# Kernel optimization log

Measured on AMD Instinct MI355X. Metric: run time of the kernel, lower is better.

Reference implementation:

```python
import jax, jax.numpy as jnp
import numpy as np

B, S, HID, H = 1, 1024, 4096, 32
DH = HID // H          # 128 head dim
DL = 2048 // H         # 64 low-rank dim per head
K = 63                 # causal conv kernel along query axis
NLAYERS = 3            # num_deep_cnn_layers
EPS = 1e-5
ROPE_BASE = 10000.0


def _layernorm(x, w, b):
    m = x.mean(-1, keepdims=True)
    v = x.var(-1, keepdims=True)
    return (x - m) * jax.lax.rsqrt(v + EPS) * w + b


def setup_inputs() -> dict:
    key = jax.random.key(0)
    ks = jax.random.split(key, 12)
    s = 0.02
    causal = jnp.tril(jnp.ones((S, S), dtype=bool))
    neg = jnp.finfo(jnp.float32).min
    return {
        "hidden_states": jax.random.normal(ks[0], (B, S, HID), jnp.float32),
        "attention_mask": jnp.broadcast_to(jnp.where(causal, 0.0, neg)[None, None], (B, 1, S, S)),
        "position_ids": jnp.broadcast_to(jnp.arange(S, dtype=jnp.int32)[None, :], (B, S)),
        "Wq": jax.random.normal(ks[1], (HID, HID), jnp.float32) * s,
        "Wk": jax.random.normal(ks[2], (HID, HID), jnp.float32) * s,
        "Wv": jax.random.normal(ks[3], (HID, HID), jnp.float32) * s,
        "Wo": jax.random.normal(ks[4], (HID, HID), jnp.float32) * s,
        "Wdq": jax.random.normal(ks[5], (DL, DH), jnp.float32) * s,  # attn_down_proj_q weight
        "Wdk": jax.random.normal(ks[6], (DL, DH), jnp.float32) * s,  # attn_down_proj_k weight
        "ln1_w": jnp.ones((S,), jnp.float32), "ln1_b": jnp.zeros((S,), jnp.float32),
        "ln2_w": jnp.ones((S,), jnp.float32), "ln2_b": jnp.zeros((S,), jnp.float32),
        "conv_w": jax.random.normal(ks[7], (NLAYERS, H, 1, K, 1), jnp.float32) / np.sqrt(K),
        "conv_b": jnp.zeros((NLAYERS, H), jnp.float32),
        "scaler_w": jax.random.normal(ks[8], (1, S), jnp.float32) * s,
        "scaler_b": jnp.zeros((1,), jnp.float32),
    }


def reference(hidden_states, attention_mask, position_ids, Wq, Wk, Wv, Wo, Wdq, Wdk,
              ln1_w, ln1_b, ln2_w, ln2_b, conv_w, conv_b, scaler_w, scaler_b):
    bsz, q_len, _ = hidden_states.shape

    def heads(x):
        return x.reshape(bsz, q_len, H, DH).transpose(0, 2, 1, 3)  # [B,H,S,DH]

    q = heads(hidden_states @ Wq.T)
    k = heads(hidden_states @ Wk.T)
    v = heads(hidden_states @ Wv.T)

    # rotary embeddings (LLaMA-style rotate_half)
    inv_freq = 1.0 / (ROPE_BASE ** (jnp.arange(0, DH, 2, dtype=jnp.float32) / DH))
    freqs = jnp.outer(jnp.arange(q_len, dtype=jnp.float32), inv_freq)
    emb = jnp.concatenate([freqs, freqs], axis=-1)             # [S,DH]
    cos = jnp.cos(emb)[position_ids][:, None]                  # [B,1,S,DH]
    sin = jnp.sin(emb)[position_ids][:, None]

    def rope(x):
        x1, x2 = jnp.split(x, 2, axis=-1)
        return x * cos + jnp.concatenate([-x2, x1], axis=-1) * sin

    q, k = rope(q), rope(k)

    # low-rank down-projection of q/k
    ql = jnp.einsum('bhsd,ed->bhse', q, Wdq)
    kl = jnp.einsum('bhsd,ed->bhse', k, Wdk)

    attn = jnp.einsum('bhqe,bhke->bhqk', ql, kl) / jnp.sqrt(jnp.float32(DL))  # [B,H,S,S]
    est_scale = jnp.einsum('bhqk,ok->bhqo', attn, scaler_w) + scaler_b       # [B,H,S,1]

    # CNN score predictor: LN -> (causal depthwise conv + ReLU) x NLAYERS -> LN
    x = _layernorm(attn, ln1_w, ln1_b)
    for i in range(NLAYERS):
        x = jax.lax.conv_general_dilated(
            x, conv_w[i], window_strides=(1, 1),
            padding=[(K - 1, 0), (0, 0)],  # causal along query axis
            dimension_numbers=('NCHW', 'OIHW', 'NCHW'),
            feature_group_count=H)
        x = jax.nn.relu(x + conv_b[i][None, :, None, None])
    x = _layernorm(x, ln2_w, ln2_b)

    x = x + attention_mask
    x = jnp.maximum(x, jnp.finfo(x.dtype).min)
    p = jax.nn.softmax(x.astype(jnp.float32), axis=-1).astype(hidden_states.dtype)
    p = p * jax.nn.sigmoid(est_scale)

    out = jnp.einsum('bhqk,bhkd->bhqd', p, v)
    out = out.transpose(0, 2, 1, 3).reshape(bsz, q_len, HID)
    return out @ Wo.T
```

## Files before the change

### kernel.cpp

```cpp
#include <hip/hip_runtime.h>
#include <hip/hip_bf16.h>

typedef __attribute__((ext_vector_type(8))) short bf16x8;
typedef __attribute__((ext_vector_type(4))) float f32x4;

#define TILE 64
#define TK 16

__device__ inline short f2bf(float x) {
    unsigned u = __float_as_uint(x);
    unsigned r = (u + 0x7fffu + ((u >> 16) & 1u)) >> 16;
    return (short)r;
}
__device__ inline float bf2f(short h) {
    return __uint_as_float(((unsigned)(unsigned short)h) << 16);
}

template<bool BT>
__global__ __launch_bounds__(256)
void gemm_f32(const float* __restrict__ A, int lda, long sA,
              const float* __restrict__ B, int ldb, long sB,
              float* __restrict__ C, int ldc, long sC,
              int M, int N, int Kd, float alpha)
{
    long bz = blockIdx.z;
    A += bz * sA; B += bz * sB; C += bz * sC;
    int m0 = blockIdx.y * TILE, n0 = blockIdx.x * TILE;
    __shared__ float As[TK][TILE + 4];
    __shared__ float Bs[TK][TILE + 4];
    int tid = threadIdx.x;
    int tm = (tid >> 4) * 4;
    int tn = (tid & 15) * 4;
    float acc[4][4] = {};
    for (int k0 = 0; k0 < Kd; k0 += TK) {
        {
            int kk = tid & 15;
            int m  = tid >> 4;
            #pragma unroll
            for (int mm = 0; mm < 4; ++mm)
                As[kk][m + mm * 16] = A[(long)(m0 + m + mm * 16) * lda + k0 + kk];
        }
        {
            int kk = tid & 15;
            int n  = tid >> 4;
            #pragma unroll
            for (int nn = 0; nn < 4; ++nn)
                Bs[kk][n + nn * 16] = B[(long)(n0 + n + nn * 16) * ldb + k0 + kk];
        }
        __syncthreads();
        #pragma unroll
        for (int kk = 0; kk < TK; ++kk) {
            float4 a4 = *reinterpret_cast<const float4*>(&As[kk][tm]);
            float4 b4 = *reinterpret_cast<const float4*>(&Bs[kk][tn]);
            float a[4] = {a4.x, a4.y, a4.z, a4.w};
            float b[4] = {b4.x, b4.y, b4.z, b4.w};
            #pragma unroll
            for (int i = 0; i < 4; ++i)
                #pragma unroll
                for (int j = 0; j < 4; ++j)
                    acc[i][j] += a[i] * b[j];
        }
        __syncthreads();
    }
    #pragma unroll
    for (int i = 0; i < 4; ++i)
        #pragma unroll
        for (int j = 0; j < 4; ++j)
            C[(long)(m0 + tm + i) * ldc + n0 + tn + j] = alpha * acc[i][j];
}

__device__ inline void gld_lds16(const __hip_bfloat16* g, __hip_bfloat16* l)
{
    __builtin_amdgcn_global_load_lds(
        (const __attribute__((address_space(1))) unsigned int*)g,
        (__attribute__((address_space(3))) unsigned int*)l,
        16, 0, 0);
}

template<int CMODE>
__global__ __launch_bounds__(256)
void gemm16(const __hip_bfloat16* __restrict__ A, int lda, long sA,
            const __hip_bfloat16* __restrict__ B, int ldb, long sB,
            void* __restrict__ Cv, int ldc, long sC,
            int Kd, float alpha)
{
    __shared__ __hip_bfloat16 As[128][32];
    __shared__ __hip_bfloat16 Bs[128][32];
    long bz = blockIdx.z;
    A += bz * sA; B += bz * sB;
    int m0 = blockIdx.y * 128, n0 = blockIdx.x * 128;
    int tid  = threadIdx.x;
    int w    = tid >> 6, lane = tid & 63;
    int wm   = w >> 1,  wn   = w & 1;
    int lrow = lane >> 2;
    int lseg = (lane & 3) * 8;
    int fr   = lane & 15;
    int kg   = (lane >> 4) * 8;
    f32x4 acc[4][4] = {};
    for (int k0 = 0; k0 < Kd; k0 += 32) {
        #pragma unroll
        for (int i = 0; i < 2; ++i) {
            int r = w * 32 + i * 16;
            gld_lds16(&A[(long)(m0 + r + lrow) * lda + k0 + lseg], &As[r][0]);
            gld_lds16(&B[(long)(n0 + r + lrow) * ldb + k0 + lseg], &Bs[r][0]);
        }
        __syncthreads();
        bf16x8 af[4], bfr[4];
        #pragma unroll
        for (int m = 0; m < 4; ++m)
            af[m] = *(const bf16x8*)&As[wm * 64 + m * 16 + fr][kg];
        #pragma unroll
        for (int n = 0; n < 4; ++n)
            bfr[n] = *(const bf16x8*)&Bs[wn * 64 + n * 16 + fr][kg];
        #pragma unroll
        for (int m = 0; m < 4; ++m)
            #pragma unroll
            for (int n = 0; n < 4; ++n)
                acc[m][n] = __builtin_amdgcn_mfma_f32_16x16x32_bf16(af[m], bfr[n], acc[m][n], 0, 0, 0);
        __syncthreads();
    }
    int crow0 = (lane >> 4) * 4;
    if constexpr (CMODE == 2) {
        __hip_bfloat16* CT = (__hip_bfloat16*)Cv + bz * sC;
        #pragma unroll
        for (int m = 0; m < 4; ++m)
            #pragma unroll
            for (int n = 0; n < 4; ++n)
                #pragma unroll
                for (int r = 0; r < 4; ++r) {
                    int row = m0 + wm * 64 + m * 16 + crow0 + r;
                    int col = n0 + wn * 64 + n * 16 + fr;
                    CT[(long)col * ldc + row] = __float2bfloat16(alpha * acc[m][n][r]);
                }
    } else {
        float* C = (float*)Cv + bz * sC;
        #pragma unroll
        for (int m = 0; m < 4; ++m)
            #pragma unroll
            for (int n = 0; n < 4; ++n)
                #pragma unroll
                for (int r = 0; r < 4; ++r) {
                    long idx = (long)(m0 + wm * 64 + m * 16 + crow0 + r) * ldc
                             + n0 + wn * 64 + n * 16 + fr;
                    float v = alpha * acc[m][n][r];
                    if constexpr (CMODE == 1) v += C[idx];
                    C[idx] = v;
                }
    }
}

__global__ __launch_bounds__(256)
void gemm16_sk(const __hip_bfloat16* __restrict__ A0, const __hip_bfloat16* __restrict__ A1,
               const __hip_bfloat16* __restrict__ A2, int lda,
               const __hip_bfloat16* __restrict__ B0, const __hip_bfloat16* __restrict__ B1,
               const __hip_bfloat16* __restrict__ B2, int ldb,
               float* __restrict__ C, int ldc,
               int kSteps, int chunksPerTerm, float alpha)
{
    __shared__ __hip_bfloat16 As[128][32];
    __shared__ __hip_bfloat16 Bs[128][32];
    int z    = blockIdx.z;
    int term = z / chunksPerTerm;
    int sub  = z - term * chunksPerTerm;
    const __hip_bfloat16* A = (term == 0) ? A0 : (term == 1) ? A1 : A2;
    const __hip_bfloat16* B = (term == 0) ? B0 : (term == 1) ? B1 : B2;
    int kbase = sub * kSteps * 32;
    int m0 = blockIdx.y * 128, n0 = blockIdx.x * 128;
    int tid  = threadIdx.x;
    int w    = tid >> 6, lane = tid & 63;
    int wm   = w >> 1,  wn   = w & 1;
    int lrow = lane >> 2;
    int lseg = (lane & 3) * 8;
    int fr   = lane & 15;
    int kg   = (lane >> 4) * 8;
    f32x4 acc[4][4] = {};
    for (int it = 0; it < kSteps; ++it) {
        int k0 = kbase + it * 32;
        #pragma unroll
        for (int i = 0; i < 2; ++i) {
            int r = w * 32 + i * 16;
            gld_lds16(&A[(long)(m0 + r + lrow) * lda + k0 + lseg], &As[r][0]);
            gld_lds16(&B[(long)(n0 + r + lrow) * ldb + k0 + lseg], &Bs[r][0]);
        }
        __syncthreads();
        bf16x8 af[4], bfr[4];
        #pragma unroll
        for (int m = 0; m < 4; ++m)
            af[m] = *(const bf16x8*)&As[wm * 64 + m * 16 + fr][kg];
        #pragma unroll
        for (int n = 0; n < 4; ++n)
            bfr[n] = *(const bf16x8*)&Bs[wn * 64 + n * 16 + fr][kg];
        #pragma unroll
        for (int m = 0; m < 4; ++m)
            #pragma unroll
            for (int n = 0; n < 4; ++n)
                acc[m][n] = __builtin_amdgcn_mfma_f32_16x16x32_bf16(af[m], bfr[n], acc[m][n], 0, 0, 0);
        __syncthreads();
    }
    int crow0 = (lane >> 4) * 4;
    #pragma unroll
    for (int m = 0; m < 4; ++m)
        #pragma unroll
        for (int n = 0; n < 4; ++n)
            #pragma unroll
            for (int r = 0; r < 4; ++r) {
                long idx = (long)(m0 + wm * 64 + m * 16 + crow0 + r) * ldc
                         + n0 + wn * 64 + n * 16 + fr;
                atomicAdd(&C[idx], alpha * acc[m][n][r]);
            }
}

#define LP 40
__global__ __launch_bounds__(256)
void gemm_s(const float* __restrict__ A, int lda, long sA,
            const float* __restrict__ B, int ldb, long sB,
            float* __restrict__ C, int ldc, long sC,
            int Kd, float alpha)
{
    __shared__ short Ah[128][LP];
    __shared__ short Bh[128][LP];
    __shared__ short Al[128][LP];
    __shared__ short Bl[128][LP];
    long bz = blockIdx.z;
    A += bz * sA; B += bz * sB; C += bz * sC;
    int m0 = blockIdx.y * 128, n0 = blockIdx.x * 128;
    int tid  = threadIdx.x;
    int lane = tid & 63;
    int w    = tid >> 6;
    int wm   = w >> 1, wn = w & 1;
    int srow = tid >> 1;
    int scol = (tid & 1) * 16;
    int fr   = lane & 15;
    int kg   = (lane >> 4) * 8;
    f32x4 acc[4][4] = {};
    for (int k0 = 0; k0 < Kd; k0 += 32) {
        #pragma unroll
        for (int ab = 0; ab < 2; ++ab) {
            const float* src = ab ? (B + (long)(n0 + srow) * ldb + k0 + scol)
                                  : (A + (long)(m0 + srow) * lda + k0 + scol);
            short* dh = ab ? &Bh[srow][scol] : &Ah[srow][scol];
            short* dl = ab ? &Bl[srow][scol] : &Al[srow][scol];
            #pragma unroll
            for (int half = 0; half < 2; ++half) {
                float4 x0 = *reinterpret_cast<const float4*>(src + half * 8);
                float4 x1 = *reinterpret_cast<const float4*>(src + half * 8 + 4);
                float xs[8] = {x0.x, x0.y, x0.z, x0.w, x1.x, x1.y, x1.z, x1.w};
                bf16x8 hv, lv;
                #pragma unroll
                for (int j = 0; j < 8; ++j) {
                    short hb = f2bf(xs[j]);
                    hv[j] = hb;
                    lv[j] = f2bf(xs[j] - bf2f(hb));
                }
                *reinterpret_cast<bf16x8*>(dh + half * 8) = hv;
                *reinterpret_cast<bf16x8*>(dl + half * 8) = lv;
            }
        }
        __syncthreads();
        bf16x8 afh[4], bfh[4], afl[4], bfl[4];
        #pragma unroll
        for (int m = 0; m < 4; ++m) {
            afh[m] = *(const bf16x8*)&Ah[wm * 64 + m * 16 + fr][kg];
            afl[m] = *(const bf16x8*)&Al[wm * 64 + m * 16 + fr][kg];
        }
        #pragma unroll
        for (int n = 0; n < 4; ++n) {
            bfh[n] = *(const bf16x8*)&Bh[wn * 64 + n * 16 + fr][kg];
            bfl[n] = *(const bf16x8*)&Bl[wn * 64 + n * 16 + fr][kg];
        }
        #pragma unroll
        for (int m = 0; m < 4; ++m)
            #pragma unroll
            for (int n = 0; n < 4; ++n) {
                acc[m][n] = __builtin_amdgcn_mfma_f32_16x16x32_bf16(afh[m], bfh[n], acc[m][n], 0, 0, 0);
                acc[m][n] = __builtin_amdgcn_mfma_f32_16x16x32_bf16(afh[m], bfl[n], acc[m][n], 0, 0, 0);
                acc[m][n] = __builtin_amdgcn_mfma_f32_16x16x32_bf16(afl[m], bfh[n], acc[m][n], 0, 0, 0);
            }
        __syncthreads();
    }
    int crow0 = (lane >> 4) * 4;
    #pragma unroll
    for (int m = 0; m < 4; ++m)
        #pragma unroll
        for (int n = 0; n < 4; ++n)
            #pragma unroll
            for (int r = 0; r < 4; ++r)
                C[(long)(m0 + wm * 64 + m * 16 + crow0 + r) * ldc
                  + n0 + wn * 64 + n * 16 + fr] = alpha * acc[m][n][r];
}

struct alignas(8) s4 { short a, b, c, d; };
template<bool LO>
__global__ __launch_bounds__(256)
void cvt_part(const float* __restrict__ x, short* __restrict__ y, long n4)
{
    long i = (long)blockIdx.x * 256 + threadIdx.x;
    long stride = (long)gridDim.x * 256;
    for (; i < n4; i += stride) {
        float4 v = reinterpret_cast<const float4*>(x)[i];
        float xs[4] = {v.x, v.y, v.z, v.w};
        s4 o;
        short* op = &o.a;
        #pragma unroll
        for (int j = 0; j < 4; ++j) {
            short hb = f2bf(xs[j]);
            op[j] = LO ? f2bf(xs[j] - bf2f(hb)) : hb;
        }
        reinterpret_cast<s4*>(y)[i] = o;
    }
}

__global__ __launch_bounds__(256)
void cvt_both(const float* __restrict__ x, short* __restrict__ yh,
              short* __restrict__ yl, long n4)
{
    long i = (long)blockIdx.x * 256 + threadIdx.x;
    long stride = (long)gridDim.x * 256;
    for (; i < n4; i += stride) {
        float4 v = reinterpret_cast<const float4*>(x)[i];
        float xs[4] = {v.x, v.y, v.z, v.w};
        s4 oh, ol;
        short* hp = &oh.a; short* lp = &ol.a;
        #pragma unroll
        for (int j = 0; j < 4; ++j) {
            short hb = f2bf(xs[j]);
            hp[j] = hb;
            lp[j] = f2bf(xs[j] - bf2f(hb));
        }
        reinterpret_cast<s4*>(yh)[i] = oh;
        reinterpret_cast<s4*>(yl)[i] = ol;
    }
}

__global__ __launch_bounds__(256)
void rope_kernel(float* __restrict__ q, float* __restrict__ k, const int* __restrict__ pos)
{
    int i = blockIdx.x * 256 + threadIdx.x;
    if (i >= 1024 * 32 * 64) return;
    int d   = i & 63;
    int rem = i >> 6;
    int h   = rem & 31;
    int s   = rem >> 5;
    float p = (float)pos[s];
    float inv = exp2f(-(float)d * (13.287712379549449f / 64.0f));
    float ang = p * inv;
    float c = cosf(ang), sn = sinf(ang);
    long base = ((long)s * 4096) + h * 128 + d;
    float x1 = q[base], x2 = q[base + 64];
    q[base]      = x1 * c - x2 * sn;
    q[base + 64] = x2 * c + x1 * sn;
    x1 = k[base]; x2 = k[base + 64];
    k[base]      = x1 * c - x2 * sn;
    k[base + 64] = x2 * c + x1 * sn;
}

__global__ __launch_bounds__(256)
void est_ln1(const float* __restrict__ x, float* __restrict__ y,
             const float* __restrict__ sw, const float* __restrict__ sbias,
             float* __restrict__ est,
             const float* __restrict__ w, const float* __restrict__ b)
{
    long row = blockIdx.x;
    const float* xr = x + row * 1024;
    float* yr = y + row * 1024;
    __shared__ float sb[12];
    float v[4];
    float s = 0.f, ss = 0.f, dt = 0.f;
    #pragma unroll
    for (int i = 0; i < 4; ++i) {
        int c = threadIdx.x + i * 256;
        v[i] = xr[c];
        s += v[i]; ss += v[i] * v[i]; dt += v[i] * sw[c];
    }
    #pragma unroll
    for (int off = 32; off; off >>= 1) {
        s  += __shfl_down(s, off, 64);
        ss += __shfl_down(ss, off, 64);
        dt += __shfl_down(dt, off, 64);
    }
    int wid = threadIdx.x >> 6, lane = threadIdx.x & 63;
    if (!lane) { sb[wid] = s; sb[4 + wid] = ss; sb[8 + wid] = dt; }
    __syncthreads();
    s  = sb[0] + sb[1] + sb[2] + sb[3];
    ss = sb[4] + sb[5] + sb[6] + sb[7];
    if (threadIdx.x == 0) est[row] = sb[8] + sb[9] + sb[10] + sb[11] + sbias[0];
    float mean = s * (1.f / 1024.f);
    float var  = ss * (1.f / 1024.f) - mean * mean;
    float inv  = rsqrtf(var + 1e-5f);
    #pragma unroll
    for (int i = 0; i < 4; ++i) {
        int c = threadIdx.x + i * 256;
        yr[c] = (v[i] - mean) * inv * w[c] + b[c];
    }
}

__global__ __launch_bounds__(256)
void conv_fast(const float* __restrict__ x, float* __restrict__ y,
               const float* __restrict__ cw, const float* __restrict__ cb,
               int layer, int h0)
{
    const int S = 1024;
    int h  = blockIdx.z;
    int hg = h0 + h;
    int q0 = blockIdx.y * 64;
    int k0 = blockIdx.x * 64;
    __shared__ float ws[63];
    if (threadIdx.x < 63) ws[threadIdx.x] = cw[(layer * 32 + hg) * 63 + threadIdx.x];
    __syncthreads();
    int c   = threadIdx.x & 63;
    int grp = threadIdx.x >> 6;
    int qb  = q0 + grp * 16;
    const float* xh = x + (long)h * S * S + k0 + c;
    float X[78];
    #pragma unroll
    for (int j = 0; j < 78; ++j) {
        int g = qb - 62 + j;
        X[j] = (g >= 0) ? xh[(long)g * S] : 0.f;
    }
    float wr[63];
    #pragma unroll
    for (int t = 0; t < 63; ++t) wr[t] = ws[t];
    float bias = cb[layer * 32 + hg];
    float* yh = y + (long)h * S * S + k0 + c;
    #pragma unroll
    for (int i = 0; i < 16; ++i) {
        float a0 = 0.f, a1 = 0.f, a2 = 0.f, a3 = 0.f;
        #pragma unroll
        for (int t = 0; t < 60; t += 4) {
            a0 += wr[t]     * X[i + t];
            a1 += wr[t + 1] * X[i + t + 1];
            a2 += wr[t + 2] * X[i + t + 2];
            a3 += wr[t + 3] * X[i + t + 3];
        }
        a0 += wr[60] * X[i + 60];
        a1 += wr[61] * X[i + 61];
        a2 += wr[62] * X[i + 62];
        float acc = bias + ((a0 + a1) + (a2 + a3));
        yh[(long)(qb + i) * S] = fmaxf(acc, 0.f);
    }
}

__global__ __launch_bounds__(256)
void ln2_softmax(const float* __restrict__ x, __hip_bfloat16* __restrict__ pb,
                 const float* __restrict__ w, const float* __restrict__ b,
                 const float* __restrict__ mask, const float* __restrict__ est)
{
    const int S = 1024;
    long row = blockIdx.x;
    int q = (int)(row & (S - 1));
    const float* xr = x + row * 1024;
    const float* mrow = mask + (long)q * S;
    __shared__ float sb[8];
    float v[4];
    float s = 0.f, ss = 0.f;
    #pragma unroll
    for (int i = 0; i < 4; ++i) {
        int c = threadIdx.x + i * 256;
        v[i] = xr[c];
        s += v[i]; ss += v[i] * v[i];
    }
    #pragma unroll
    for (int off = 32; off; off >>= 1) {
        s  += __shfl_down(s, off, 64);
        ss += __shfl_down(ss, off, 64);
    }
    int wid = threadIdx.x >> 6, lane = threadIdx.x & 63;
    if (!lane) { sb[wid] = s; sb[4 + wid] = ss; }
    __syncthreads();
    s  = sb[0] + sb[1] + sb[2] + sb[3];
    ss = sb[4] + sb[5] + sb[6] + sb[7];
    float mean = s * (1.f / 1024.f);
    float var  = ss * (1.f / 1024.f) - mean * mean;
    float inv  = rsqrtf(var + 1e-5f);
    const float FMIN = -3.4028235e38f;
    float mx = FMIN;
    #pragma unroll
    for (int i = 0; i < 4; ++i) {
        int c = threadIdx.x + i * 256;
        float t = (v[i] - mean) * inv * w[c] + b[c] + mrow[c];
        t = fmaxf(t, FMIN);
        v[i] = t;
        mx = fmaxf(mx, t);
    }
    #pragma unroll
    for (int off = 32; off; off >>= 1) mx = fmaxf(mx, __shfl_down(mx, off, 64));
    __syncthreads();
    if (!lane) sb[wid] = mx;
    __syncthreads();
    mx = fmaxf(fmaxf(sb[0], sb[1]), fmaxf(sb[2], sb[3]));
    float s2 = 0.f;
    #pragma unroll
    for (int i = 0; i < 4; ++i) { v[i] = expf(v[i] - mx); s2 += v[i]; }
    #pragma unroll
    for (int off = 32; off; off >>= 1) s2 += __shfl_down(s2, off, 64);
    __syncthreads();
    if (!lane) sb[4 + wid] = s2;
    __syncthreads();
    s2 = sb[4] + sb[5] + sb[6] + sb[7];
    float e = est[row];
    float sc = (1.f / (1.f + expf(-e))) / s2;
    __hip_bfloat16* pr = pb + row * S;
    #pragma unroll
    for (int i = 0; i < 4; ++i) {
        int c = threadIdx.x + i * 256;
        pr[c] = __float2bfloat16(v[i] * sc);
    }
}

extern "C" void kernel_launch(void* const* d_in, const int* in_sizes, int n_in,
                              void* d_out, int out_size, void* d_ws, size_t ws_size,
                              hipStream_t stream) {
    const int S = 1024, H = 32, HID = 4096, DH = 128, DL = 64;

    const float* hs   = (const float*)d_in[0];
    const float* mask = (const float*)d_in[1];
    const int*   pos  = (const int*)d_in[2];
    const float* Wq   = (const float*)d_in[3];
    const float* Wk   = (const float*)d_in[4];
    const float* Wv   = (const float*)d_in[5];
    const float* Wo   = (const float*)d_in[6];
    const float* Wdq  = (const float*)d_in[7];
    const float* Wdk  = (const float*)d_in[8];
    const float* ln1w = (const float*)d_in[9];
    const float* ln1b = (const float*)d_in[10];
    const float* ln2w = (const float*)d_in[11];
    const float* ln2b = (const float*)d_in[12];
    const float* cw   = (const float*)d_in[13];
    const float* cb   = (const float*)d_in[14];
    const float* sw   = (const float*)d_in[15];
    const float* sbia = (const float*)d_in[16];
    float* out = (float*)d_out;

    float* p   = (float*)d_ws;
    float* qb  = p; p += (long)S * HID;
    float* kb  = p; p += (long)S * HID;
    float* ql  = p; p += (long)H * S * DL;
    float* kl  = p; p += (long)H * S * DL;
    float* est = p; p += (long)H * S;
    short* hsH = (short*)p; p += (long)S * HID / 2;
    short* hsL = (short*)p; p += (long)S * HID / 2;
    short* Wb  = (short*)p; p += (long)HID * HID / 2;
    short* WbL = (short*)p; p += (long)HID * HID / 2;
    float* ao  = qb;
    short* aoH = hsH;
    short* vT  = hsL;

    long wsFloats  = (long)(ws_size / 4);
    long usedFixed = p - (float*)d_ws;
    long perHead   = 2L * S * S;
    int CH = (int)((wsFloats - usedFixed) / perHead);
    if (CH > H) CH = H;
    if (CH < 1) CH = 1;
    float* sc0 = p;
    float* sc1 = sc0 + (long)CH * S * S;
    __hip_bfloat16* pb = (__hip_bfloat16*)sc1;

    dim3 blk(256);
    long n4_hs = (long)S * HID / 4, n4_W = (long)HID * HID / 4;
    size_t projBytes = (size_t)S * HID * sizeof(float);

    cvt_both<<<2048, blk, 0, stream>>>(hs, hsH, hsL, n4_hs);

    hipMemsetAsync(qb, 0, projBytes, stream);
    cvt_both<<<2048, blk, 0, stream>>>(Wq, Wb, WbL, n4_W);
    gemm16_sk<<<dim3(HID / 128, S / 128, 6), blk, 0, stream>>>(
        (__hip_bfloat16*)hsH, (__hip_bfloat16*)hsL, (__hip_bfloat16*)hsH, HID,
        (__hip_bfloat16*)Wb,  (__hip_bfloat16*)Wb,  (__hip_bfloat16*)WbL, HID,
        qb, HID, 64, 2, 1.f);

    hipMemsetAsync(kb, 0, projBytes, stream);
    cvt_both<<<2048, blk, 0, stream>>>(Wk, Wb, WbL, n4_W);
    gemm16_sk<<<dim3(HID / 128, S / 128, 6), blk, 0, stream>>>(
        (__hip_bfloat16*)hsH, (__hip_bfloat16*)hsL, (__hip_bfloat16*)hsH, HID,
        (__hip_bfloat16*)Wb,  (__hip_bfloat16*)Wb,  (__hip_bfloat16*)WbL, HID,
        kb, HID, 64, 2, 1.f);

    cvt_part<false><<<2048, blk, 0, stream>>>(Wv, Wb, n4_W);
    gemm16<2><<<dim3(HID / 128, S / 128, 1), blk, 0, stream>>>(
        (__hip_bfloat16*)hsH, HID, 0, (__hip_bfloat16*)Wb, HID, 0, vT, S, 0, HID, 1.f);

    rope_kernel<<<(S * H * 64 + 255) / 256, blk, 0, stream>>>(qb, kb, pos);

    gemm_f32<true><<<dim3(1, S / 64, H), blk, 0, stream>>>(qb, HID, 128, Wdq, DH, 0, ql, DL, (long)S * DL, S, DL, DH, 1.f);
    gemm_f32<true><<<dim3(1, S / 64, H), blk, 0, stream>>>(kb, HID, 128, Wdk, DH, 0, kl, DL, (long)S * DL, S, DL, DH, 1.f);

    for (int c0 = 0; c0 < H; c0 += CH) {
        int ch = (c0 + CH <= H) ? CH : (H - c0);
        gemm_s<<<dim3(S / 128, S / 128, ch), blk, 0, stream>>>(
            ql + (long)c0 * S * DL, DL, (long)S * DL,
            kl + (long)c0 * S * DL, DL, (long)S * DL,
            sc0, S, (long)S * S, DL, 0.125f);
        est_ln1<<<ch * S, blk, 0, stream>>>(sc0, sc1, sw, sbia, est + (long)c0 * S, ln1w, ln1b);
        conv_fast<<<dim3(16, 16, ch), blk, 0, stream>>>(sc1, sc0, cw, cb, 0, c0);
        conv_fast<<<dim3(16, 16, ch), blk, 0, stream>>>(sc0, sc1, cw, cb, 1, c0);
        conv_fast<<<dim3(16, 16, ch), blk, 0, stream>>>(sc1, sc0, cw, cb, 2, c0);
        ln2_softmax<<<ch * S, blk, 0, stream>>>(sc0, pb, ln2w, ln2b, mask, est + (long)c0 * S);
        gemm16<0><<<dim3(1, S / 128, ch), blk, 0, stream>>>(
            (__hip_bfloat16*)pb, S, (long)S * S,
            (__hip_bfloat16*)(vT + (long)c0 * DH * S), S, (long)DH * S,
            ao + (long)c0 * 128, HID, 128,
            S, 1.f);
    }

    cvt_part<false><<<2048, blk, 0, stream>>>(ao, aoH, n4_hs);
    cvt_part<false><<<2048, blk, 0, stream>>>(Wo, Wb, n4_W);
    hipMemsetAsync(out, 0, projBytes, stream);
    gemm16_sk<<<dim3(HID / 128, S / 128, 2), blk, 0, stream>>>(
        (__hip_bfloat16*)aoH, (__hip_bfloat16*)aoH, (__hip_bfloat16*)aoH, HID,
        (__hip_bfloat16*)Wb,  (__hip_bfloat16*)Wb,  (__hip_bfloat16*)Wb,  HID,
        out, HID, 64, 2, 1.f);
}
```

Before: 1.147 ms.

## Split-K projections deeper, route V through split-K plus transpose, emit bf16 attention output

The Q/K projection split-K factor doubles, giving more K-chunks and more blocks. The V projection moves from a single-slice transposed-store GEMM to a split-K GEMM into fp32 followed by a new shared-memory transpose kernel. The P·V GEMM now writes bf16 directly through a new epilogue mode, which removes the separate fp32-to-bf16 conversion pass before the output projection. These changes aim to fill more CUs on the skinny GEMMs and cut a memory pass, in exchange for extra atomic accumulation traffic and one added transpose kernel.

```diff
diff --git a/kernel.cpp b/kernel.cpp
--- a/kernel.cpp
+++ b/kernel.cpp
@@ -132,6 +132,16 @@
                     int col = n0 + wn * 64 + n * 16 + fr;
                     CT[(long)col * ldc + row] = __float2bfloat16(alpha * acc[m][n][r]);
                 }
+    } else if constexpr (CMODE == 3) {
+        __hip_bfloat16* C = (__hip_bfloat16*)Cv + bz * sC;
+        #pragma unroll
+        for (int m = 0; m < 4; ++m)
+            #pragma unroll
+            for (int n = 0; n < 4; ++n)
+                #pragma unroll
+                for (int r = 0; r < 4; ++r)
+                    C[(long)(m0 + wm * 64 + m * 16 + crow0 + r) * ldc
+                      + n0 + wn * 64 + n * 16 + fr] = __float2bfloat16(alpha * acc[m][n][r]);
     } else {
         float* C = (float*)Cv + bz * sC;
         #pragma unroll
@@ -333,6 +343,20 @@
 }
 
 __global__ __launch_bounds__(256)
+void transpose_v(const float* __restrict__ v, __hip_bfloat16* __restrict__ vT)
+{
+    __shared__ __hip_bfloat16 t[64][65];
+    int h = blockIdx.z, s0 = blockIdx.x * 64, d0 = blockIdx.y * 64;
+    int c = threadIdx.x & 63, r = threadIdx.x >> 6;
+    for (int i = r; i < 64; i += 4)
+        t[i][c] = __float2bfloat16(v[(long)(s0 + i) * 4096 + h * 128 + d0 + c]);
+    __syncthreads();
+    __hip_bfloat16* o = vT + ((long)h * 128 + d0) * 1024 + s0;
+    for (int i = r; i < 64; i += 4)
+        o[(long)i * 1024 + c] = t[c][i];
+}
+
+__global__ __launch_bounds__(256)
 void rope_kernel(float* __restrict__ q, float* __restrict__ k, const int* __restrict__ pos)
 {
     int i = blockIdx.x * 256 + threadIdx.x;
@@ -541,7 +565,6 @@
     short* hsL = (short*)p; p += (long)S * HID / 2;
     short* Wb  = (short*)p; p += (long)HID * HID / 2;
     short* WbL = (short*)p; p += (long)HID * HID / 2;
-    float* ao  = qb;
     short* aoH = hsH;
     short* vT  = hsL;
 
@@ -563,26 +586,30 @@
 
     hipMemsetAsync(qb, 0, projBytes, stream);
     cvt_both<<<2048, blk, 0, stream>>>(Wq, Wb, WbL, n4_W);
-    gemm16_sk<<<dim3(HID / 128, S / 128, 6), blk, 0, stream>>>(
+    gemm16_sk<<<dim3(HID / 128, S / 128, 12), blk, 0, stream>>>(
         (__hip_bfloat16*)hsH, (__hip_bfloat16*)hsL, (__hip_bfloat16*)hsH, HID,
         (__hip_bfloat16*)Wb,  (__hip_bfloat16*)Wb,  (__hip_bfloat16*)WbL, HID,
-        qb, HID, 64, 2, 1.f);
+        qb, HID, 32, 4, 1.f);
 
     hipMemsetAsync(kb, 0, projBytes, stream);
     cvt_both<<<2048, blk, 0, stream>>>(Wk, Wb, WbL, n4_W);
-    gemm16_sk<<<dim3(HID / 128, S / 128, 6), blk, 0, stream>>>(
+    gemm16_sk<<<dim3(HID / 128, S / 128, 12), blk, 0, stream>>>(
         (__hip_bfloat16*)hsH, (__hip_bfloat16*)hsL, (__hip_bfloat16*)hsH, HID,
         (__hip_bfloat16*)Wb,  (__hip_bfloat16*)Wb,  (__hip_bfloat16*)WbL, HID,
-        kb, HID, 64, 2, 1.f);
-
-    cvt_part<false><<<2048, blk, 0, stream>>>(Wv, Wb, n4_W);
-    gemm16<2><<<dim3(HID / 128, S / 128, 1), blk, 0, stream>>>(
-        (__hip_bfloat16*)hsH, HID, 0, (__hip_bfloat16*)Wb, HID, 0, vT, S, 0, HID, 1.f);
+        kb, HID, 32, 4, 1.f);
 
     rope_kernel<<<(S * H * 64 + 255) / 256, blk, 0, stream>>>(qb, kb, pos);
 
     gemm_f32<true><<<dim3(1, S / 64, H), blk, 0, stream>>>(qb, HID, 128, Wdq, DH, 0, ql, DL, (long)S * DL, S, DL, DH, 1.f);
     gemm_f32<true><<<dim3(1, S / 64, H), blk, 0, stream>>>(kb, HID, 128, Wdk, DH, 0, kl, DL, (long)S * DL, S, DL, DH, 1.f);
+
+    hipMemsetAsync(qb, 0, projBytes, stream);
+    cvt_part<false><<<2048, blk, 0, stream>>>(Wv, Wb, n4_W);
+    gemm16_sk<<<dim3(HID / 128, S / 128, 4), blk, 0, stream>>>(
+        (__hip_bfloat16*)hsH, (__hip_bfloat16*)hsH, (__hip_bfloat16*)hsH, HID,
+        (__hip_bfloat16*)Wb,  (__hip_bfloat16*)Wb,  (__hip_bfloat16*)Wb,  HID,
+        qb, HID, 32, 4, 1.f);
+    transpose_v<<<dim3(S / 64, DH / 64, H), blk, 0, stream>>>(qb, (__hip_bfloat16*)vT);
 
     for (int c0 = 0; c0 < H; c0 += CH) {
         int ch = (c0 + CH <= H) ? CH : (H - c0);
@@ -595,18 +622,17 @@
         conv_fast<<<dim3(16, 16, ch), blk, 0, stream>>>(sc0, sc1, cw, cb, 1, c0);
         conv_fast<<<dim3(16, 16, ch), blk, 0, stream>>>(sc1, sc0, cw, cb, 2, c0);
         ln2_softmax<<<ch * S, blk, 0, stream>>>(sc0, pb, ln2w, ln2b, mask, est + (long)c0 * S);
-        gemm16<0><<<dim3(1, S / 128, ch), blk, 0, stream>>>(
+        gemm16<3><<<dim3(1, S / 128, ch), blk, 0, stream>>>(
             (__hip_bfloat16*)pb, S, (long)S * S,
             (__hip_bfloat16*)(vT + (long)c0 * DH * S), S, (long)DH * S,
-            ao + (long)c0 * 128, HID, 128,
+            aoH + (long)c0 * 128, HID, 128,
             S, 1.f);
     }
 
-    cvt_part<false><<<2048, blk, 0, stream>>>(ao, aoH, n4_hs);
     cvt_part<false><<<2048, blk, 0, stream>>>(Wo, Wb, n4_W);
     hipMemsetAsync(out, 0, projBytes, stream);
-    gemm16_sk<<<dim3(HID / 128, S / 128, 2), blk, 0, stream>>>(
+    gemm16_sk<<<dim3(HID / 128, S / 128, 4), blk, 0, stream>>>(
         (__hip_bfloat16*)aoH, (__hip_bfloat16*)aoH, (__hip_bfloat16*)aoH, HID,
         (__hip_bfloat16*)Wb,  (__hip_bfloat16*)Wb,  (__hip_bfloat16*)Wb,  HID,
-        out, HID, 64, 2, 1.f);
-}
+        out, HID, 32, 4, 1.f);
+}
```

Result: slower. 1.311 ms (+14.3%).

## Fold LN1 into first conv, write attention output as bf16, retune split-K

Applied to the files above, without the earlier changes.

The first layernorm is no longer a separate pass that writes a normalized SxS tensor. A stats kernel now emits per-row scale and offset, and the first conv layer applies the normalization while loading its input. This removes one full read/write of each head's score matrix. The PV GEMM gains a bf16 row-major output mode that writes straight into the bf16 buffer for the output projection, removing a conversion kernel. The Q/K projection split-K count drops from 6 to 3 with a larger k-chunk. The trade-off is that the conv reloads the LN stats per element and uses more registers.

```diff
diff --git a/kernel.cpp b/kernel.cpp
--- a/kernel.cpp
+++ b/kernel.cpp
@@ -132,6 +132,16 @@
                     int col = n0 + wn * 64 + n * 16 + fr;
                     CT[(long)col * ldc + row] = __float2bfloat16(alpha * acc[m][n][r]);
                 }
+    } else if constexpr (CMODE == 3) {
+        __hip_bfloat16* C = (__hip_bfloat16*)Cv + bz * sC;
+        #pragma unroll
+        for (int m = 0; m < 4; ++m)
+            #pragma unroll
+            for (int n = 0; n < 4; ++n)
+                #pragma unroll
+                for (int r = 0; r < 4; ++r)
+                    C[(long)(m0 + wm * 64 + m * 16 + crow0 + r) * ldc
+                      + n0 + wn * 64 + n * 16 + fr] = __float2bfloat16(alpha * acc[m][n][r]);
     } else {
         float* C = (float*)Cv + bz * sC;
         #pragma unroll
@@ -355,22 +365,19 @@
 }
 
 __global__ __launch_bounds__(256)
-void est_ln1(const float* __restrict__ x, float* __restrict__ y,
-             const float* __restrict__ sw, const float* __restrict__ sbias,
-             float* __restrict__ est,
-             const float* __restrict__ w, const float* __restrict__ b)
+void row_stats(const float* __restrict__ x,
+               const float* __restrict__ sw, const float* __restrict__ sbias,
+               float* __restrict__ est, float* __restrict__ lnA, float* __restrict__ lnO)
 {
     long row = blockIdx.x;
     const float* xr = x + row * 1024;
-    float* yr = y + row * 1024;
     __shared__ float sb[12];
-    float v[4];
     float s = 0.f, ss = 0.f, dt = 0.f;
     #pragma unroll
     for (int i = 0; i < 4; ++i) {
         int c = threadIdx.x + i * 256;
-        v[i] = xr[c];
-        s += v[i]; ss += v[i] * v[i]; dt += v[i] * sw[c];
+        float v = xr[c];
+        s += v; ss += v * v; dt += v * sw[c];
     }
     #pragma unroll
     for (int off = 32; off; off >>= 1) {
@@ -381,16 +388,70 @@
     int wid = threadIdx.x >> 6, lane = threadIdx.x & 63;
     if (!lane) { sb[wid] = s; sb[4 + wid] = ss; sb[8 + wid] = dt; }
     __syncthreads();
-    s  = sb[0] + sb[1] + sb[2] + sb[3];
-    ss = sb[4] + sb[5] + sb[6] + sb[7];
-    if (threadIdx.x == 0) est[row] = sb[8] + sb[9] + sb[10] + sb[11] + sbias[0];
-    float mean = s * (1.f / 1024.f);
-    float var  = ss * (1.f / 1024.f) - mean * mean;
-    float inv  = rsqrtf(var + 1e-5f);
-    #pragma unroll
-    for (int i = 0; i < 4; ++i) {
-        int c = threadIdx.x + i * 256;
-        yr[c] = (v[i] - mean) * inv * w[c] + b[c];
+    if (threadIdx.x == 0) {
+        s  = sb[0] + sb[1] + sb[2] + sb[3];
+        ss = sb[4] + sb[5] + sb[6] + sb[7];
+        float mean = s * (1.f / 1024.f);
+        float var  = ss * (1.f / 1024.f) - mean * mean;
+        float a    = rsqrtf(var + 1e-5f);
+        est[row] = sb[8] + sb[9] + sb[10] + sb[11] + sbias[0];
+        lnA[row] = a;
+        lnO[row] = -mean * a;
+    }
+}
+
+__global__ __launch_bounds__(256)
+void conv_ln1(const float* __restrict__ x, float* __restrict__ y,
+              const float* __restrict__ cw, const float* __restrict__ cb,
+              const float* __restrict__ lnA, const float* __restrict__ lnO,
+              const float* __restrict__ w1, const float* __restrict__ b1, int h0)
+{
+    const int S = 1024;
+    int h  = blockIdx.z;
+    int hg = h0 + h;
+    int q0 = blockIdx.y * 64;
+    int k0 = blockIdx.x * 64;
+    __shared__ float ws[63];
+    if (threadIdx.x < 63) ws[threadIdx.x] = cw[hg * 63 + threadIdx.x];
+    __syncthreads();
+    int c   = threadIdx.x & 63;
+    int grp = threadIdx.x >> 6;
+    int qb  = q0 + grp * 16;
+    float wc = w1[k0 + c];
+    float bc = b1[k0 + c];
+    const float* xh = x + (long)h * S * S + k0 + c;
+    const float* lA = lnA + (long)h * S;
+    const float* lO = lnO + (long)h * S;
+    float X[78];
+    #pragma unroll
+    for (int j = 0; j < 78; ++j) {
+        int g = qb - 62 + j;
+        if (g >= 0) {
+            float a = lA[g], o = lO[g];
+            float raw = xh[(long)g * S];
+            X[j] = fmaf(raw * a + o, wc, bc);
+        } else X[j] = 0.f;
+    }
+    float wr[63];
+    #pragma unroll
+    for (int t = 0; t < 63; ++t) wr[t] = ws[t];
+    float bias = cb[hg];
+    float* yh = y + (long)h * S * S + k0 + c;
+    #pragma unroll
+    for (int i = 0; i < 16; ++i) {
+        float a0 = 0.f, a1 = 0.f, a2 = 0.f, a3 = 0.f;
+        #pragma unroll
+        for (int t = 0; t < 60; t += 4) {
+            a0 += wr[t]     * X[i + t];
+            a1 += wr[t + 1] * X[i + t + 1];
+            a2 += wr[t + 2] * X[i + t + 2];
+            a3 += wr[t + 3] * X[i + t + 3];
+        }
+        a0 += wr[60] * X[i + 60];
+        a1 += wr[61] * X[i + 61];
+        a2 += wr[62] * X[i + 62];
+        float acc = bias + ((a0 + a1) + (a2 + a3));
+        yh[(long)(qb + i) * S] = fmaxf(acc, 0.f);
     }
 }
 
@@ -537,11 +598,12 @@
     float* ql  = p; p += (long)H * S * DL;
     float* kl  = p; p += (long)H * S * DL;
     float* est = p; p += (long)H * S;
+    float* lnA = p; p += (long)H * S;
+    float* lnO = p; p += (long)H * S;
     short* hsH = (short*)p; p += (long)S * HID / 2;
     short* hsL = (short*)p; p += (long)S * HID / 2;
     short* Wb  = (short*)p; p += (long)HID * HID / 2;
     short* WbL = (short*)p; p += (long)HID * HID / 2;
-    float* ao  = qb;
     short* aoH = hsH;
     short* vT  = hsL;
 
@@ -553,7 +615,7 @@
     if (CH < 1) CH = 1;
     float* sc0 = p;
     float* sc1 = sc0 + (long)CH * S * S;
-    __hip_bfloat16* pb = (__hip_bfloat16*)sc1;
+    __hip_bfloat16* pb = (__hip_bfloat16*)sc0;
 
     dim3 blk(256);
     long n4_hs = (long)S * HID / 4, n4_W = (long)HID * HID / 4;
@@ -563,17 +625,17 @@
 
     hipMemsetAsync(qb, 0, projBytes, stream);
     cvt_both<<<2048, blk, 0, stream>>>(Wq, Wb, WbL, n4_W);
-    gemm16_sk<<<dim3(HID / 128, S / 128, 6), blk, 0, stream>>>(
+    gemm16_sk<<<dim3(HID / 128, S / 128, 3), blk, 0, stream>>>(
         (__hip_bfloat16*)hsH, (__hip_bfloat16*)hsL, (__hip_bfloat16*)hsH, HID,
         (__hip_bfloat16*)Wb,  (__hip_bfloat16*)Wb,  (__hip_bfloat16*)WbL, HID,
-        qb, HID, 64, 2, 1.f);
+        qb, HID, 128, 1, 1.f);
 
     hipMemsetAsync(kb, 0, projBytes, stream);
     cvt_both<<<2048, blk, 0, stream>>>(Wk, Wb, WbL, n4_W);
-    gemm16_sk<<<dim3(HID / 128, S / 128, 6), blk, 0, stream>>>(
+    gemm16_sk<<<dim3(HID / 128, S / 128, 3), blk, 0, stream>>>(
         (__hip_bfloat16*)hsH, (__hip_bfloat16*)hsL, (__hip_bfloat16*)hsH, HID,
         (__hip_bfloat16*)Wb,  (__hip_bfloat16*)Wb,  (__hip_bfloat16*)WbL, HID,
-        kb, HID, 64, 2, 1.f);
+        kb, HID, 128, 1, 1.f);
 
     cvt_part<false><<<2048, blk, 0, stream>>>(Wv, Wb, n4_W);
     gemm16<2><<<dim3(HID / 128, S / 128, 1), blk, 0, stream>>>(
@@ -590,19 +652,20 @@
             ql + (long)c0 * S * DL, DL, (long)S * DL,
             kl + (long)c0 * S * DL, DL, (long)S * DL,
             sc0, S, (long)S * S, DL, 0.125f);
-        est_ln1<<<ch * S, blk, 0, stream>>>(sc0, sc1, sw, sbia, est + (long)c0 * S, ln1w, ln1b);
-        conv_fast<<<dim3(16, 16, ch), blk, 0, stream>>>(sc1, sc0, cw, cb, 0, c0);
-        conv_fast<<<dim3(16, 16, ch), blk, 0, stream>>>(sc0, sc1, cw, cb, 1, c0);
-        conv_fast<<<dim3(16, 16, ch), blk, 0, stream>>>(sc1, sc0, cw, cb, 2, c0);
-        ln2_softmax<<<ch * S, blk, 0, stream>>>(sc0, pb, ln2w, ln2b, mask, est + (long)c0 * S);
-        gemm16<0><<<dim3(1, S / 128, ch), blk, 0, stream>>>(
+        row_stats<<<ch * S, blk, 0, stream>>>(sc0, sw, sbia,
+            est + (long)c0 * S, lnA + (long)c0 * S, lnO + (long)c0 * S);
+        conv_ln1<<<dim3(16, 16, ch), blk, 0, stream>>>(sc0, sc1, cw, cb,
+            lnA + (long)c0 * S, lnO + (long)c0 * S, ln1w, ln1b, c0);
+        conv_fast<<<dim3(16, 16, ch), blk, 0, stream>>>(sc1, sc0, cw, cb, 1, c0);
+        conv_fast<<<dim3(16, 16, ch), blk, 0, stream>>>(sc0, sc1, cw, cb, 2, c0);
+        ln2_softmax<<<ch * S, blk, 0, stream>>>(sc1, pb, ln2w, ln2b, mask, est + (long)c0 * S);
+        gemm16<3><<<dim3(1, S / 128, ch), blk, 0, stream>>>(
             (__hip_bfloat16*)pb, S, (long)S * S,
             (__hip_bfloat16*)(vT + (long)c0 * DH * S), S, (long)DH * S,
-            ao + (long)c0 * 128, HID, 128,
+            aoH + (long)c0 * 128, HID, 128,
             S, 1.f);
     }
 
-    cvt_part<false><<<2048, blk, 0, stream>>>(ao, aoH, n4_hs);
     cvt_part<false><<<2048, blk, 0, stream>>>(Wo, Wb, n4_W);
     hipMemsetAsync(out, 0, projBytes, stream);
     gemm16_sk<<<dim3(HID / 128, S / 128, 2), blk, 0, stream>>>(
```

Measured after the change: 1.298 ms. 1.13x slower.
